# Kernel tuning notes

Hardware: AMD Instinct MI355X
Metric: run time of the kernel (lower is better)

Reference implementation:

```python
import jax, jax.numpy as jnp
import numpy as np

B = 128      # number of swarms
NA = 64      # agents per swarm (na)
D = 8        # input feature dim
RD = 128     # attention hidden dim r
H = 16       # output channels h (l = sqrt(h) = 4)


def setup_inputs() -> dict:
    key = jax.random.key(0)
    ks = jax.random.split(key, 16)
    x = jax.random.normal(ks[0], (B * NA, D, NA), dtype=jnp.float32)
    L = jax.random.randint(ks[1], (B * NA, D, NA), 0, 2).astype(jnp.float32)
    p = lambda k, shp: jax.random.normal(k, shp, dtype=jnp.float32)
    return {
        "x": x, "L": L,
        "Aq": p(ks[2], (RD, D)), "Ak": p(ks[3], (RD, D)), "Av": p(ks[4], (RD, D)),
        "Aq1": p(ks[5], (RD, RD)), "Ak1": p(ks[6], (RD, RD)), "Av1": p(ks[7], (RD, RD)),
        "Aq5": p(ks[8], (RD, RD)), "Ak5": p(ks[9], (RD, RD)), "Av5": p(ks[10], (RD, RD)),
        "Ao": p(ks[11], (RD, RD)), "Ao1": p(ks[12], (RD, RD)), "Ao5": p(ks[13], (H, RD)),
    }


def _attn(Xin, Aq, Ak, Av, sqrt_nn):
    # Xin: (b, f, n); Aq/Ak/Av: (r, f); sqrt_nn: (b, 1, 1)
    Q = jax.nn.sigmoid(jnp.einsum('rf,bfn->bnr', Aq, Xin))   # Q already transposed
    K = jax.nn.sigmoid(jnp.einsum('rf,bfn->brn', Ak, Xin))
    V = jax.nn.sigmoid(jnp.einsum('rf,bfn->bnr', Av, Xin))
    S = jnp.einsum('bnr,brm->bnm', Q, K) / sqrt_nn           # (b, n, n)
    A = jax.nn.softmax(S, axis=2)
    return jnp.einsum('bnm,bmr->brn', A, V)                  # o^T: (b, r, n)


def _kron_eye2(A):
    # torch.kron(A, eye(2)) per batch: (B, n, n) -> (B, 2n, 2n)
    Bq, n, _ = A.shape
    I2 = jnp.eye(2, dtype=A.dtype)
    return (A[:, :, None, :, None] * I2[None, :, None, :]).reshape(Bq, 2 * n, 2 * n)


def reference(x, L, Aq, Ak, Av, Aq1, Ak1, Av1, Aq5, Ak5, Av5, Ao, Ao1, Ao5):
    na = x.shape[2]
    Bsw = x.shape[0] // na
    num_nb = jnp.sum((L[:, 0, :] >= 1.0).astype(jnp.float32), axis=1) + 1.0
    sqrt_nn = jnp.sqrt(num_nb)[:, None, None]                # (Bx, 1, 1)

    o = _attn(x, Aq, Ak, Av, sqrt_nn)
    R = jax.nn.silu(jnp.einsum('sr,brn->bsn', Ao, o))
    o = _attn(R, Aq1, Ak1, Av1, sqrt_nn)
    R = jax.nn.silu(jnp.einsum('sr,brn->bsn', Ao1, o))
    o = _attn(R, Aq5, Ak5, Av5, sqrt_nn)
    R = jax.nn.silu(jnp.einsum('hr,brn->bhn', Ao5, o))       # (Bx, 16, na)

    blk = lambda a, b: R[:, a:b, :].sum(axis=1).reshape(Bsw, na, na)
    R11 = _kron_eye2(blk(0, 4))
    R12 = _kron_eye2(blk(4, 8))
    R21 = _kron_eye2(blk(8, 12))
    R22 = _kron_eye2(blk(12, 16))
    # block matrix [[R11, R12], [R21, R22]] -> (Bsw, 4na, 4na)
    Rfull = jnp.concatenate(
        (jnp.concatenate((R11, R21), axis=1), jnp.concatenate((R12, R22), axis=1)),
        axis=2)

    Rfull = Rfull ** 2
    Rupper = Rfull + jnp.swapaxes(Rfull, 1, 2)
    n_tot = 4 * na
    Dg = jnp.eye(n_tot, dtype=Rupper.dtype)
    Rdiag = Rupper * (1.0 - Dg)                              # diag zeroed
    Rout = Dg * Rupper                                       # keep diag only
    rowsum = jnp.sum(Rdiag, axis=2)[:, :, None]              # (Bsw, n, 1)
    return Rout + Dg * rowsum - Rdiag
```

## Files before the change

kernel.cpp:

```cpp
#include <hip/hip_runtime.h>
#include <hip/hip_bf16.h>

typedef _Float16 f16;
typedef __attribute__((ext_vector_type(8))) _Float16 h8v;
typedef __attribute__((ext_vector_type(4))) float f4v;
typedef __attribute__((ext_vector_type(16))) float f16acc;

#define OFF_WQ  0
#define OFF_WK  2048
#define OFF_WV  4096
#define OFF_AQ1 6144
#define OFF_AK1 22528
#define OFF_AV1 38912
#define OFF_AQ5 55296
#define OFF_AK5 71680
#define OFF_AV5 88064
#define OFF_AO  104448
#define OFF_AO1 120832
#define OFF_AO5 137216
#define WTS_TOTAL 139264

__device__ __forceinline__ f4v mfma16_(h8v a, h8v b, f4v c) {
  return __builtin_amdgcn_mfma_f32_16x16x32_f16(a, b, c, 0, 0, 0);
}
__device__ __forceinline__ f16acc mfma32_(h8v a, h8v b, f16acc c) {
  return __builtin_amdgcn_mfma_f32_32x32x16_f16(a, b, c, 0, 0, 0);
}
__device__ __forceinline__ float rcp_(float x) { return __builtin_amdgcn_rcpf(x); }
__device__ __forceinline__ unsigned int pk2(float a, float b) {
  __fp16 __attribute__((ext_vector_type(2))) h2 = __builtin_amdgcn_cvt_pkrtz(a, b);
  return *reinterpret_cast<unsigned int*>(&h2);
}
__device__ __forceinline__ f16acc zero16() {
  f16acc z;
  #pragma unroll
  for (int i = 0; i < 16; ++i) z[i] = 0.f;
  return z;
}

__device__ __forceinline__ f16* swz256(f16* b, int n, int k) {
  int byte = (n << 8) + (k << 1); byte ^= (n & 7) << 4;
  return (f16*)((char*)b + byte);
}
__device__ __forceinline__ const f16* swz256c(const f16* b, int n, int k) {
  int byte = (n << 8) + (k << 1); byte ^= (n & 7) << 4;
  return (const f16*)((const char*)b + byte);
}
__device__ __forceinline__ f16* swz128(f16* b, int r, int m) {
  int byte = (r << 7) + (m << 1); byte ^= (r & 7) << 4;
  return (f16*)((char*)b + byte);
}
__device__ __forceinline__ const f16* swz128c(const f16* b, int r, int m) {
  int byte = (r << 7) + (m << 1); byte ^= (r & 7) << 4;
  return (const f16*)((const char*)b + byte);
}

template<int ACT>
__device__ __forceinline__ unsigned long long pack4act(f4v acc) {
  float v[4];
  #pragma unroll
  for (int j = 0; j < 4; ++j) {
    float t = acc[j];
    if (ACT == 0)      t = rcp_(1.0f + __expf(-t));
    else if (ACT == 1) t = t * rcp_(1.0f + __expf(-t));
    v[j] = t;
  }
  union { unsigned long long u64; unsigned int u32[2]; } u;
  u.u32[0] = pk2(v[0], v[1]);
  u.u32[1] = pk2(v[2], v[3]);
  return u.u64;
}

template<int NKK>
__device__ __forceinline__ void mm_qkv(const f16* __restrict__ Wq,
                                       const f16* __restrict__ Wk,
                                       const f16* __restrict__ Wv,
                                       const f16* __restrict__ Xt,
                                       f16* __restrict__ Qt, f16* __restrict__ Kt,
                                       f16* __restrict__ Vb, int w, int lane)
{
  const int l31 = lane & 31, lh = lane >> 5;
  const int rt = w >> 1, ct = w & 1;
  h8v xf[NKK];
  #pragma unroll
  for (int kk = 0; kk < NKK; ++kk)
    xf[kk] = *(const h8v*)swz256c(Xt, ct * 32 + l31, kk * 16 + lh * 8);
  f16acc aq = zero16(), ak = zero16(), av = zero16();
  #pragma unroll
  for (int kk = 0; kk < NKK; ++kk) {
    const int fo = (rt * NKK + kk) * 512 + lane * 8;
    h8v fq = *(const h8v*)(Wq + fo);
    h8v fk = *(const h8v*)(Wk + fo);
    h8v fv = *(const h8v*)(Wv + fo);
    aq = mfma32_(fq, xf[kk], aq);
    ak = mfma32_(fk, xf[kk], ak);
    av = mfma32_(xf[kk], fv, av);
  }
  const int n = ct * 32 + l31;
  #pragma unroll
  for (int q = 0; q < 4; ++q) {
    const int rr = rt * 32 + q * 8 + lh * 4;
    f4v t;
    t = (f4v){aq[4*q], aq[4*q+1], aq[4*q+2], aq[4*q+3]};
    *(unsigned long long*)swz256(Qt, n, rr) = pack4act<0>(t);
    t = (f4v){ak[4*q], ak[4*q+1], ak[4*q+2], ak[4*q+3]};
    *(unsigned long long*)swz256(Kt, n, rr) = pack4act<0>(t);
    t = (f4v){av[4*q], av[4*q+1], av[4*q+2], av[4*q+3]};
    *(unsigned long long*)swz128(Vb, rt * 32 + l31, ct * 32 + q * 8 + lh * 4) = pack4act<0>(t);
  }
}

__device__ __forceinline__ void mm_pv32(const f16* __restrict__ Vb,
                                        const f16* __restrict__ Ps,
                                        f16* __restrict__ Ot, int w, int lane)
{
  const int l31 = lane & 31, lh = lane >> 5;
  const int rt = w >> 1, ct = w & 1;
  f16acc acc = zero16();
  #pragma unroll
  for (int kk = 0; kk < 4; ++kk) {
    h8v a = *(const h8v*)swz128c(Vb, rt * 32 + l31, kk * 16 + lh * 8);
    h8v b = *(const h8v*)swz128c(Ps, ct * 32 + l31, kk * 16 + lh * 8);
    acc = mfma32_(a, b, acc);
  }
  const int n = ct * 32 + l31;
  #pragma unroll
  for (int q = 0; q < 4; ++q) {
    f4v t = (f4v){acc[4*q], acc[4*q+1], acc[4*q+2], acc[4*q+3]};
    *(unsigned long long*)swz256(Ot, n, rt * 32 + q * 8 + lh * 4) = pack4act<2>(t);
  }
}

__device__ __forceinline__ void mm_ao32(const f16* __restrict__ Ao,
                                        const f16* __restrict__ Ot,
                                        f16* __restrict__ Rt, int w, int lane)
{
  const int l31 = lane & 31, lh = lane >> 5;
  const int st = w >> 1, ct = w & 1;
  f16acc acc = zero16();
  #pragma unroll
  for (int kk = 0; kk < 8; ++kk) {
    h8v a = *(const h8v*)(Ao + (st * 8 + kk) * 512 + lane * 8);
    h8v b = *(const h8v*)swz256c(Ot, ct * 32 + l31, kk * 16 + lh * 8);
    acc = mfma32_(a, b, acc);
  }
  const int n = ct * 32 + l31;
  #pragma unroll
  for (int q = 0; q < 4; ++q) {
    f4v t = (f4v){acc[4*q], acc[4*q+1], acc[4*q+2], acc[4*q+3]};
    *(unsigned long long*)swz256(Rt, n, st * 32 + q * 8 + lh * 4) = pack4act<1>(t);
  }
}

__device__ __forceinline__ void s_softmax(const f16* __restrict__ QtL,
                                          const f16* __restrict__ KtL,
                                          f16* __restrict__ PsL,
                                          float is, int w, int lane)
{
  const int lrow = lane & 15, lk = lane >> 4;
  const int n = 16 * w + lrow;
  h8v bq[4];
  #pragma unroll
  for (int kk = 0; kk < 4; ++kk)
    bq[kk] = *(const h8v*)swz256c(QtL, n, kk * 32 + lk * 8);
  f4v acc[4];
  #pragma unroll
  for (int mt = 0; mt < 4; ++mt) {
    acc[mt] = (f4v){0.f, 0.f, 0.f, 0.f};
    #pragma unroll
    for (int kk = 0; kk < 4; ++kk) {
      h8v ak = *(const h8v*)swz256c(KtL, mt * 16 + lrow, kk * 32 + lk * 8);
      acc[mt] = mfma16_(ak, bq[kk], acc[mt]);
    }
  }
  float mx = -1e30f;
  #pragma unroll
  for (int mt = 0; mt < 4; ++mt)
    #pragma unroll
    for (int j = 0; j < 4; ++j) { acc[mt][j] *= is; mx = fmaxf(mx, acc[mt][j]); }
  mx = fmaxf(mx, __shfl_xor(mx, 16));
  mx = fmaxf(mx, __shfl_xor(mx, 32));
  float sm = 0.f;
  #pragma unroll
  for (int mt = 0; mt < 4; ++mt)
    #pragma unroll
    for (int j = 0; j < 4; ++j) { acc[mt][j] = __expf(acc[mt][j] - mx); sm += acc[mt][j]; }
  sm += __shfl_xor(sm, 16);
  sm += __shfl_xor(sm, 32);
  const float inv = rcp_(sm);
  #pragma unroll
  for (int mt = 0; mt < 4; ++mt) {
    union { unsigned long long u64; unsigned int u32[2]; } u;
    u.u32[0] = pk2(acc[mt][0] * inv, acc[mt][1] * inv);
    u.u32[1] = pk2(acc[mt][2] * inv, acc[mt][3] * inv);
    *(unsigned long long*)swz128(PsL, n, mt * 16 + lk * 4) = u.u64;
  }
}

__device__ __forceinline__ void mm_final(const f16* __restrict__ Ao5g,
                                         const f16* __restrict__ OtL,
                                         float* __restrict__ rch_b, int w, int lane)
{
  const int lrow = lane & 15, lk = lane >> 4;
  h8v a[4];
  #pragma unroll
  for (int kk = 0; kk < 4; ++kk)
    a[kk] = *(const h8v*)(Ao5g + lrow * 128 + kk * 32 + lk * 8);
  const int n = 16 * w + lrow;
  f4v acc = {0.f, 0.f, 0.f, 0.f};
  #pragma unroll
  for (int kk = 0; kk < 4; ++kk) {
    h8v b = *(const h8v*)swz256c(OtL, n, kk * 32 + lk * 8);
    acc = mfma16_(a[kk], b, acc);
  }
  #pragma unroll
  for (int j = 0; j < 4; ++j) {
    float v = acc[j];
    v = v * rcp_(1.0f + __expf(-v));
    rch_b[(lk * 4 + j) * 64 + n] = v;
  }
}

__global__ __launch_bounds__(512, 4)
void swarm_attn_mfma(const float* __restrict__ x, const float* __restrict__ L,
                     const f16* __restrict__ wts, float* __restrict__ rch)
{
  __shared__ f16 Xt[64 * 128];
  __shared__ f16 Qt[64 * 128];
  __shared__ f16 Kt[64 * 128];
  __shared__ f16 Vb[128 * 64];
  __shared__ f16 Ps[64 * 64];
  __shared__ float s_inv;

  const int b = blockIdx.x;
  const int tid = threadIdx.x;
  const int w = tid >> 6, lane = tid & 63;

  {
    const int n = tid >> 3, c = tid & 7;
    unsigned int val = 0;
    if (c < 4) {
      const float a  = x[(size_t)b * 512 + (2 * c) * 64 + n];
      const float bb = x[(size_t)b * 512 + (2 * c + 1) * 64 + n];
      val = pk2(a, bb);
    }
    *(unsigned int*)swz256(Xt, n, 2 * c) = val;
  }
  if (w == 0) {
    const float lv = L[(size_t)b * 512 + lane];
    const unsigned long long msk = __ballot(lv >= 1.0f);
    if (lane == 0) s_inv = __frsqrt_rn((float)(__popcll(msk) + 1));
  }
  __syncthreads();
  const float is = s_inv;

  mm_qkv<1>(wts + OFF_WQ, wts + OFF_WK, wts + OFF_WV, Xt, Qt, Kt, Vb, w, lane);
  __syncthreads();
  if (w < 4) s_softmax(Qt, Kt, Ps, is, w, lane);
  __syncthreads();
  mm_pv32(Vb, Ps, Qt, w, lane);
  __syncthreads();
  mm_ao32(wts + OFF_AO, Qt, Xt, w, lane);
  __syncthreads();

  mm_qkv<8>(wts + OFF_AQ1, wts + OFF_AK1, wts + OFF_AV1, Xt, Qt, Kt, Vb, w, lane);
  __syncthreads();
  if (w < 4) s_softmax(Qt, Kt, Ps, is, w, lane);
  __syncthreads();
  mm_pv32(Vb, Ps, Qt, w, lane);
  __syncthreads();
  mm_ao32(wts + OFF_AO1, Qt, Xt, w, lane);
  __syncthreads();

  mm_qkv<8>(wts + OFF_AQ5, wts + OFF_AK5, wts + OFF_AV5, Xt, Qt, Kt, Vb, w, lane);
  __syncthreads();
  if (w < 4) s_softmax(Qt, Kt, Ps, is, w, lane);
  __syncthreads();
  mm_pv32(Vb, Ps, Qt, w, lane);
  __syncthreads();
  if (w < 4) mm_final(wts + OFF_AO5, Qt, rch + (size_t)b * 1024, w, lane);
}

__global__ void conv_wts(const float* Aq, const float* Ak, const float* Av,
                         const float* Aq1, const float* Ak1, const float* Av1,
                         const float* Aq5, const float* Ak5, const float* Av5,
                         const float* Ao, const float* Ao1, const float* Ao5,
                         f16* wts)
{
  const int t = blockIdx.x * 256 + threadIdx.x;
  if (t >= WTS_TOTAL) return;
  float v;
  if (t < 6144) {
    const int m = t >> 11, idx = t & 2047;
    const int fi = idx >> 9, rem = idx & 511, lane = rem >> 3, j = rem & 7;
    const int r = fi * 32 + (lane & 31), k = (lane >> 5) * 8 + j;
    const float* W = (m == 0) ? Aq : (m == 1) ? Ak : Av;
    v = (k < 8) ? W[r * 8 + k] : 0.f;
  } else if (t < 137216) {
    const int m = (t - 6144) >> 14, idx = (t - 6144) & 16383;
    const int fi = idx >> 9, rem = idx & 511, lane = rem >> 3, j = rem & 7;
    const int rt = fi >> 3, kk = fi & 7;
    const int r = rt * 32 + (lane & 31), k = kk * 16 + (lane >> 5) * 8 + j;
    const float* W = (m == 0) ? Aq1 : (m == 1) ? Ak1 : (m == 2) ? Av1 :
                     (m == 3) ? Aq5 : (m == 4) ? Ak5 : (m == 5) ? Av5 :
                     (m == 6) ? Ao : Ao1;
    v = W[r * 128 + k];
  } else {
    v = Ao5[t - 137216];
  }
  wts[t] = (f16)v;
}

#define ASTR 65
__global__ __launch_bounds__(256, 1)
void reduce_kernel(const float* __restrict__ rch, float* __restrict__ Mw,
                   float* __restrict__ rsw, float* __restrict__ csw)
{
  __shared__ float Msh[4 * 64 * ASTR];
  const int s = blockIdx.x, t = threadIdx.x;
  for (int e = t; e < 16384; e += 256) {
    const int j = e & 63, i = (e >> 6) & 63, g = e >> 12;
    const float* p = rch + ((size_t)s * 64 + i) * 1024 + (4 * g) * 64 + j;
    const float v = p[0] + p[64] + p[128] + p[192];
    Msh[(g * 64 + i) * ASTR + j] = v;
    Mw[(size_t)s * 16384 + e] = v;
  }
  __syncthreads();
  const int g = t >> 6, i = t & 63;
  float r2 = 0.f, c2 = 0.f;
  for (int j = 0; j < 64; ++j) {
    const float a = Msh[(g * 64 + i) * ASTR + j];
    const float bb = Msh[(g * 64 + j) * ASTR + i];
    r2 = fmaf(a, a, r2);
    c2 = fmaf(bb, bb, c2);
  }
  rsw[s * 256 + g * 64 + i] = r2;
  csw[s * 256 + g * 64 + i] = c2;
}

__global__ __launch_bounds__(256, 1)
void expand_kernel(const float* __restrict__ Mw, const float* __restrict__ rsw,
                   const float* __restrict__ csw, float* __restrict__ out)
{
  const size_t e = ((size_t)blockIdx.x * 256 + threadIdx.x) * 4;
  const int s = (int)(e >> 16);
  const int rem = (int)(e & 65535);
  const int u = rem >> 8, v0 = rem & 255;
  const int ub = u >> 7, ii = (u & 127) >> 1, p = u & 1;
  const float* Ms = Mw + (size_t)s * 16384;
  float4 o;
  float* po = &o.x;
  #pragma unroll
  for (int c = 0; c < 4; ++c) {
    const int v = v0 + c;
    const int vb = v >> 7, jj = (v & 127) >> 1, q = v & 1;
    float val = 0.f;
    if (u == v) {
      val = rsw[s * 256 + (2 * ub) * 64 + ii] + rsw[s * 256 + (2 * ub + 1) * 64 + ii]
          + csw[s * 256 + ub * 64 + ii] + csw[s * 256 + (2 + ub) * 64 + ii];
    } else if (p == q) {
      const int g = 2 * ub + vb, gp = 2 * vb + ub;
      const float a = Ms[g * 4096 + ii * 64 + jj];
      const float bb = Ms[gp * 4096 + jj * 64 + ii];
      val = -(a * a + bb * bb);
    }
    po[c] = val;
  }
  *(float4*)(out + e) = o;
}

extern "C" void kernel_launch(void* const* d_in, const int* in_sizes, int n_in,
                              void* d_out, int out_size, void* d_ws, size_t ws_size,
                              hipStream_t stream)
{
  const float* x   = (const float*)d_in[0];
  const float* L   = (const float*)d_in[1];
  const float* Aq  = (const float*)d_in[2];
  const float* Ak  = (const float*)d_in[3];
  const float* Av  = (const float*)d_in[4];
  const float* Aq1 = (const float*)d_in[5];
  const float* Ak1 = (const float*)d_in[6];
  const float* Av1 = (const float*)d_in[7];
  const float* Aq5 = (const float*)d_in[8];
  const float* Ak5 = (const float*)d_in[9];
  const float* Av5 = (const float*)d_in[10];
  const float* Ao  = (const float*)d_in[11];
  const float* Ao1 = (const float*)d_in[12];
  const float* Ao5 = (const float*)d_in[13];

  f16* wts = (f16*)d_ws;
  float* Mw  = (float*)((char*)d_ws + (size_t)WTS_TOTAL * 2);
  float* rsw = Mw + (size_t)128 * 16384;
  float* csw = rsw + 128 * 256;
  float* rch = (float*)d_out;

  conv_wts<<<(WTS_TOTAL + 255) / 256, 256, 0, stream>>>(Aq, Ak, Av, Aq1, Ak1, Av1,
                                                        Aq5, Ak5, Av5, Ao, Ao1, Ao5, wts);
  swarm_attn_mfma<<<8192, 512, 0, stream>>>(x, L, wts, rch);
  reduce_kernel<<<128, 256, 0, stream>>>(rch, Mw, rsw, csw);
  expand_kernel<<<8192, 256, 0, stream>>>(Mw, rsw, csw, (float*)d_out);
}
```

Before: 332.2 us.

## Keep per-wave activations in registers with 16x16x16 MFMA tiling

Restructures the attention kernel so each of 4 waves owns 16 agents and keeps Q, P, O and the next-layer input in registers as 16x16x16 MFMA fragments. Only K and V go through shared memory, which removes the Xt/Qt/Ps buffers and about half the barriers per layer. Weights are repacked for the new fragment layout. In exchange it uses the older 16x16x16 MFMA with half the K depth, issues more MFMA instructions, and runs 256-thread blocks with higher register pressure.

After: 573.2 us. 1.73x slower.

```diff
diff --git a/kernel.cpp b/kernel.cpp
--- a/kernel.cpp
+++ b/kernel.cpp
@@ -1,10 +1,9 @@
 #include <hip/hip_runtime.h>
-#include <hip/hip_bf16.h>
 
 typedef _Float16 f16;
+typedef __attribute__((ext_vector_type(4))) _Float16 h4v;
 typedef __attribute__((ext_vector_type(8))) _Float16 h8v;
 typedef __attribute__((ext_vector_type(4))) float f4v;
-typedef __attribute__((ext_vector_type(16))) float f16acc;
 
 #define OFF_WQ  0
 #define OFF_WK  2048
@@ -20,23 +19,14 @@
 #define OFF_AO5 137216
 #define WTS_TOTAL 139264
 
-__device__ __forceinline__ f4v mfma16_(h8v a, h8v b, f4v c) {
-  return __builtin_amdgcn_mfma_f32_16x16x32_f16(a, b, c, 0, 0, 0);
-}
-__device__ __forceinline__ f16acc mfma32_(h8v a, h8v b, f16acc c) {
-  return __builtin_amdgcn_mfma_f32_32x32x16_f16(a, b, c, 0, 0, 0);
+__device__ __forceinline__ f4v mfma_(h4v a, h4v b, f4v c) {
+  return __builtin_amdgcn_mfma_f32_16x16x16f16(a, b, c, 0, 0, 0);
 }
 __device__ __forceinline__ float rcp_(float x) { return __builtin_amdgcn_rcpf(x); }
 __device__ __forceinline__ unsigned int pk2(float a, float b) {
   __fp16 __attribute__((ext_vector_type(2))) h2 = __builtin_amdgcn_cvt_pkrtz(a, b);
   return *reinterpret_cast<unsigned int*>(&h2);
 }
-__device__ __forceinline__ f16acc zero16() {
-  f16acc z;
-  #pragma unroll
-  for (int i = 0; i < 16; ++i) z[i] = 0.f;
-  return z;
-}
 
 __device__ __forceinline__ f16* swz256(f16* b, int n, int k) {
   int byte = (n << 8) + (k << 1); byte ^= (n & 7) << 4;
@@ -55,8 +45,10 @@
   return (const f16*)((const char*)b + byte);
 }
 
+union pkun { unsigned long long u64; unsigned int u32[2]; h4v h; };
+
 template<int ACT>
-__device__ __forceinline__ unsigned long long pack4act(f4v acc) {
+__device__ __forceinline__ pkun pack4act(f4v acc) {
   float v[4];
   #pragma unroll
   for (int j = 0; j < 4; ++j) {
@@ -65,112 +57,67 @@
     else if (ACT == 1) t = t * rcp_(1.0f + __expf(-t));
     v[j] = t;
   }
-  union { unsigned long long u64; unsigned int u32[2]; } u;
+  pkun u;
   u.u32[0] = pk2(v[0], v[1]);
   u.u32[1] = pk2(v[2], v[3]);
-  return u.u64;
-}
-
-template<int NKK>
-__device__ __forceinline__ void mm_qkv(const f16* __restrict__ Wq,
-                                       const f16* __restrict__ Wk,
-                                       const f16* __restrict__ Wv,
-                                       const f16* __restrict__ Xt,
-                                       f16* __restrict__ Qt, f16* __restrict__ Kt,
-                                       f16* __restrict__ Vb, int w, int lane)
-{
-  const int l31 = lane & 31, lh = lane >> 5;
-  const int rt = w >> 1, ct = w & 1;
-  h8v xf[NKK];
-  #pragma unroll
-  for (int kk = 0; kk < NKK; ++kk)
-    xf[kk] = *(const h8v*)swz256c(Xt, ct * 32 + l31, kk * 16 + lh * 8);
-  f16acc aq = zero16(), ak = zero16(), av = zero16();
-  #pragma unroll
-  for (int kk = 0; kk < NKK; ++kk) {
-    const int fo = (rt * NKK + kk) * 512 + lane * 8;
-    h8v fq = *(const h8v*)(Wq + fo);
-    h8v fk = *(const h8v*)(Wk + fo);
-    h8v fv = *(const h8v*)(Wv + fo);
-    aq = mfma32_(fq, xf[kk], aq);
-    ak = mfma32_(fk, xf[kk], ak);
-    av = mfma32_(xf[kk], fv, av);
-  }
-  const int n = ct * 32 + l31;
-  #pragma unroll
-  for (int q = 0; q < 4; ++q) {
-    const int rr = rt * 32 + q * 8 + lh * 4;
-    f4v t;
-    t = (f4v){aq[4*q], aq[4*q+1], aq[4*q+2], aq[4*q+3]};
-    *(unsigned long long*)swz256(Qt, n, rr) = pack4act<0>(t);
-    t = (f4v){ak[4*q], ak[4*q+1], ak[4*q+2], ak[4*q+3]};
-    *(unsigned long long*)swz256(Kt, n, rr) = pack4act<0>(t);
-    t = (f4v){av[4*q], av[4*q+1], av[4*q+2], av[4*q+3]};
-    *(unsigned long long*)swz128(Vb, rt * 32 + l31, ct * 32 + q * 8 + lh * 4) = pack4act<0>(t);
-  }
-}
-
-__device__ __forceinline__ void mm_pv32(const f16* __restrict__ Vb,
-                                        const f16* __restrict__ Ps,
-                                        f16* __restrict__ Ot, int w, int lane)
-{
-  const int l31 = lane & 31, lh = lane >> 5;
-  const int rt = w >> 1, ct = w & 1;
-  f16acc acc = zero16();
-  #pragma unroll
-  for (int kk = 0; kk < 4; ++kk) {
-    h8v a = *(const h8v*)swz128c(Vb, rt * 32 + l31, kk * 16 + lh * 8);
-    h8v b = *(const h8v*)swz128c(Ps, ct * 32 + l31, kk * 16 + lh * 8);
-    acc = mfma32_(a, b, acc);
-  }
-  const int n = ct * 32 + l31;
-  #pragma unroll
-  for (int q = 0; q < 4; ++q) {
-    f4v t = (f4v){acc[4*q], acc[4*q+1], acc[4*q+2], acc[4*q+3]};
-    *(unsigned long long*)swz256(Ot, n, rt * 32 + q * 8 + lh * 4) = pack4act<2>(t);
-  }
-}
-
-__device__ __forceinline__ void mm_ao32(const f16* __restrict__ Ao,
-                                        const f16* __restrict__ Ot,
-                                        f16* __restrict__ Rt, int w, int lane)
-{
-  const int l31 = lane & 31, lh = lane >> 5;
-  const int st = w >> 1, ct = w & 1;
-  f16acc acc = zero16();
-  #pragma unroll
-  for (int kk = 0; kk < 8; ++kk) {
-    h8v a = *(const h8v*)(Ao + (st * 8 + kk) * 512 + lane * 8);
-    h8v b = *(const h8v*)swz256c(Ot, ct * 32 + l31, kk * 16 + lh * 8);
-    acc = mfma32_(a, b, acc);
-  }
-  const int n = ct * 32 + l31;
-  #pragma unroll
-  for (int q = 0; q < 4; ++q) {
-    f4v t = (f4v){acc[4*q], acc[4*q+1], acc[4*q+2], acc[4*q+3]};
-    *(unsigned long long*)swz256(Rt, n, st * 32 + q * 8 + lh * 4) = pack4act<1>(t);
-  }
-}
-
-__device__ __forceinline__ void s_softmax(const f16* __restrict__ QtL,
-                                          const f16* __restrict__ KtL,
-                                          f16* __restrict__ PsL,
-                                          float is, int w, int lane)
-{
-  const int lrow = lane & 15, lk = lane >> 4;
-  const int n = 16 * w + lrow;
-  h8v bq[4];
-  #pragma unroll
-  for (int kk = 0; kk < 4; ++kk)
-    bq[kk] = *(const h8v*)swz256c(QtL, n, kk * 32 + lk * 8);
+  return u;
+}
+
+__device__ __forceinline__ h4v lo4(h8v p) { return __builtin_shufflevector(p, p, 0, 1, 2, 3); }
+__device__ __forceinline__ h4v hi4(h8v p) { return __builtin_shufflevector(p, p, 4, 5, 6, 7); }
+
+template<int NF>
+__device__ __forceinline__ void qkv_phase(const f16* __restrict__ Wq,
+                                          const f16* __restrict__ Wk,
+                                          const f16* __restrict__ Wv,
+                                          const h4v* __restrict__ xf,
+                                          h4v* __restrict__ qreg,
+                                          f16* __restrict__ Kt, f16* __restrict__ Vb,
+                                          int lane, int n, int lrow, int lk, int s0)
+{
+  #pragma unroll
+  for (int rt = 0; rt < 8; ++rt) {
+    f4v aq = {0.f,0.f,0.f,0.f}, ak = {0.f,0.f,0.f,0.f}, av = {0.f,0.f,0.f,0.f};
+    if (NF == 1) {
+      h4v fq = *(const h4v*)(Wq + rt * 256 + lane * 4);
+      h4v fk = *(const h4v*)(Wk + rt * 256 + lane * 4);
+      h4v fv = *(const h4v*)(Wv + rt * 256 + lane * 4);
+      aq = mfma_(fq, xf[0], aq);
+      ak = mfma_(fk, xf[0], ak);
+      av = mfma_(xf[0], fv, av);
+    } else {
+      #pragma unroll
+      for (int kp = 0; kp < NF / 2; ++kp) {
+        h8v pq = *(const h8v*)(Wq + (rt * 4 + kp) * 512 + lane * 8);
+        h8v pk = *(const h8v*)(Wk + (rt * 4 + kp) * 512 + lane * 8);
+        h8v pv = *(const h8v*)(Wv + (rt * 4 + kp) * 512 + lane * 8);
+        aq = mfma_(lo4(pq), xf[2 * kp], aq);
+        aq = mfma_(hi4(pq), xf[2 * kp + 1], aq);
+        ak = mfma_(lo4(pk), xf[2 * kp], ak);
+        ak = mfma_(hi4(pk), xf[2 * kp + 1], ak);
+        av = mfma_(xf[2 * kp], lo4(pv), av);
+        av = mfma_(xf[2 * kp + 1], hi4(pv), av);
+      }
+    }
+    qreg[rt] = pack4act<0>(aq).h;
+    *(unsigned long long*)swz256(Kt, n, rt * 16 + lk * 4) = pack4act<0>(ak).u64;
+    *(unsigned long long*)swz128(Vb, rt * 16 + lrow, s0 + lk * 4) = pack4act<0>(av).u64;
+  }
+}
+
+__device__ __forceinline__ void softmax_phase(const f16* __restrict__ Kt,
+                                              const h4v* __restrict__ qreg,
+                                              h4v* __restrict__ preg,
+                                              float is, int lrow, int lk)
+{
   f4v acc[4];
   #pragma unroll
   for (int mt = 0; mt < 4; ++mt) {
     acc[mt] = (f4v){0.f, 0.f, 0.f, 0.f};
     #pragma unroll
-    for (int kk = 0; kk < 4; ++kk) {
-      h8v ak = *(const h8v*)swz256c(KtL, mt * 16 + lrow, kk * 32 + lk * 8);
-      acc[mt] = mfma16_(ak, bq[kk], acc[mt]);
+    for (int kr = 0; kr < 8; ++kr) {
+      h4v a = *(const h4v*)swz256c(Kt, mt * 16 + lrow, kr * 16 + lk * 4);
+      acc[mt] = mfma_(a, qreg[kr], acc[mt]);
     }
   }
   float mx = -1e30f;
@@ -190,95 +137,108 @@
   const float inv = rcp_(sm);
   #pragma unroll
   for (int mt = 0; mt < 4; ++mt) {
-    union { unsigned long long u64; unsigned int u32[2]; } u;
+    pkun u;
     u.u32[0] = pk2(acc[mt][0] * inv, acc[mt][1] * inv);
     u.u32[1] = pk2(acc[mt][2] * inv, acc[mt][3] * inv);
-    *(unsigned long long*)swz128(PsL, n, mt * 16 + lk * 4) = u.u64;
-  }
-}
-
-__device__ __forceinline__ void mm_final(const f16* __restrict__ Ao5g,
-                                         const f16* __restrict__ OtL,
-                                         float* __restrict__ rch_b, int w, int lane)
-{
-  const int lrow = lane & 15, lk = lane >> 4;
-  h8v a[4];
-  #pragma unroll
-  for (int kk = 0; kk < 4; ++kk)
-    a[kk] = *(const h8v*)(Ao5g + lrow * 128 + kk * 32 + lk * 8);
-  const int n = 16 * w + lrow;
-  f4v acc = {0.f, 0.f, 0.f, 0.f};
-  #pragma unroll
-  for (int kk = 0; kk < 4; ++kk) {
-    h8v b = *(const h8v*)swz256c(OtL, n, kk * 32 + lk * 8);
-    acc = mfma16_(a[kk], b, acc);
-  }
-  #pragma unroll
-  for (int j = 0; j < 4; ++j) {
-    float v = acc[j];
-    v = v * rcp_(1.0f + __expf(-v));
-    rch_b[(lk * 4 + j) * 64 + n] = v;
-  }
-}
-
-__global__ __launch_bounds__(512, 4)
+    preg[mt] = u.h;
+  }
+}
+
+__device__ __forceinline__ void pv_phase(const f16* __restrict__ Vb,
+                                         const h4v* __restrict__ preg,
+                                         h4v* __restrict__ oreg, int lrow, int lk)
+{
+  #pragma unroll
+  for (int rt = 0; rt < 8; ++rt) {
+    f4v acc = {0.f, 0.f, 0.f, 0.f};
+    #pragma unroll
+    for (int km = 0; km < 4; ++km) {
+      h4v a = *(const h4v*)swz128c(Vb, rt * 16 + lrow, km * 16 + lk * 4);
+      acc = mfma_(a, preg[km], acc);
+    }
+    oreg[rt] = pack4act<2>(acc).h;
+  }
+}
+
+__device__ __forceinline__ void ao_phase(const f16* __restrict__ Ao,
+                                         const h4v* __restrict__ oreg,
+                                         h4v* __restrict__ xf, int lane)
+{
+  #pragma unroll
+  for (int st = 0; st < 8; ++st) {
+    f4v acc = {0.f, 0.f, 0.f, 0.f};
+    #pragma unroll
+    for (int kp = 0; kp < 4; ++kp) {
+      h8v pa = *(const h8v*)(Ao + (st * 4 + kp) * 512 + lane * 8);
+      acc = mfma_(lo4(pa), oreg[2 * kp], acc);
+      acc = mfma_(hi4(pa), oreg[2 * kp + 1], acc);
+    }
+    xf[st] = pack4act<1>(acc).h;
+  }
+}
+
+__global__ __launch_bounds__(256, 4)
 void swarm_attn_mfma(const float* __restrict__ x, const float* __restrict__ L,
                      const f16* __restrict__ wts, float* __restrict__ rch)
 {
-  __shared__ f16 Xt[64 * 128];
-  __shared__ f16 Qt[64 * 128];
   __shared__ f16 Kt[64 * 128];
   __shared__ f16 Vb[128 * 64];
-  __shared__ f16 Ps[64 * 64];
   __shared__ float s_inv;
 
-  const int b = blockIdx.x;
-  const int tid = threadIdx.x;
+  const int b = blockIdx.x, tid = threadIdx.x;
   const int w = tid >> 6, lane = tid & 63;
+  const int lrow = lane & 15, lk = lane >> 4;
+  const int s0 = w * 16;
+  const int n = s0 + lrow;
+
+  h4v xf[8], qreg[8], preg[4], oreg[8];
+
+  #pragma unroll
+  for (int j = 0; j < 4; ++j) {
+    const int f = lk * 4 + j;
+    xf[0][j] = (f < 8) ? (f16)x[(size_t)b * 512 + f * 64 + n] : (f16)0.f;
+  }
+  if (tid < 64) {
+    const float lv = L[(size_t)b * 512 + tid];
+    const unsigned long long msk = __ballot(lv >= 1.0f);
+    if (tid == 0) s_inv = __frsqrt_rn((float)(__popcll(msk) + 1));
+  }
+
+  qkv_phase<1>(wts + OFF_WQ, wts + OFF_WK, wts + OFF_WV, xf, qreg, Kt, Vb, lane, n, lrow, lk, s0);
+  __syncthreads();
+  const float is = s_inv;
+  softmax_phase(Kt, qreg, preg, is, lrow, lk);
+  pv_phase(Vb, preg, oreg, lrow, lk);
+  __syncthreads();
+  ao_phase(wts + OFF_AO, oreg, xf, lane);
+
+  qkv_phase<8>(wts + OFF_AQ1, wts + OFF_AK1, wts + OFF_AV1, xf, qreg, Kt, Vb, lane, n, lrow, lk, s0);
+  __syncthreads();
+  softmax_phase(Kt, qreg, preg, is, lrow, lk);
+  pv_phase(Vb, preg, oreg, lrow, lk);
+  __syncthreads();
+  ao_phase(wts + OFF_AO1, oreg, xf, lane);
+
+  qkv_phase<8>(wts + OFF_AQ5, wts + OFF_AK5, wts + OFF_AV5, xf, qreg, Kt, Vb, lane, n, lrow, lk, s0);
+  __syncthreads();
+  softmax_phase(Kt, qreg, preg, is, lrow, lk);
+  pv_phase(Vb, preg, oreg, lrow, lk);
 
   {
-    const int n = tid >> 3, c = tid & 7;
-    unsigned int val = 0;
-    if (c < 4) {
-      const float a  = x[(size_t)b * 512 + (2 * c) * 64 + n];
-      const float bb = x[(size_t)b * 512 + (2 * c + 1) * 64 + n];
-      val = pk2(a, bb);
-    }
-    *(unsigned int*)swz256(Xt, n, 2 * c) = val;
-  }
-  if (w == 0) {
-    const float lv = L[(size_t)b * 512 + lane];
-    const unsigned long long msk = __ballot(lv >= 1.0f);
-    if (lane == 0) s_inv = __frsqrt_rn((float)(__popcll(msk) + 1));
-  }
-  __syncthreads();
-  const float is = s_inv;
-
-  mm_qkv<1>(wts + OFF_WQ, wts + OFF_WK, wts + OFF_WV, Xt, Qt, Kt, Vb, w, lane);
-  __syncthreads();
-  if (w < 4) s_softmax(Qt, Kt, Ps, is, w, lane);
-  __syncthreads();
-  mm_pv32(Vb, Ps, Qt, w, lane);
-  __syncthreads();
-  mm_ao32(wts + OFF_AO, Qt, Xt, w, lane);
-  __syncthreads();
-
-  mm_qkv<8>(wts + OFF_AQ1, wts + OFF_AK1, wts + OFF_AV1, Xt, Qt, Kt, Vb, w, lane);
-  __syncthreads();
-  if (w < 4) s_softmax(Qt, Kt, Ps, is, w, lane);
-  __syncthreads();
-  mm_pv32(Vb, Ps, Qt, w, lane);
-  __syncthreads();
-  mm_ao32(wts + OFF_AO1, Qt, Xt, w, lane);
-  __syncthreads();
-
-  mm_qkv<8>(wts + OFF_AQ5, wts + OFF_AK5, wts + OFF_AV5, Xt, Qt, Kt, Vb, w, lane);
-  __syncthreads();
-  if (w < 4) s_softmax(Qt, Kt, Ps, is, w, lane);
-  __syncthreads();
-  mm_pv32(Vb, Ps, Qt, w, lane);
-  __syncthreads();
-  if (w < 4) mm_final(wts + OFF_AO5, Qt, rch + (size_t)b * 1024, w, lane);
+    f4v acc = {0.f, 0.f, 0.f, 0.f};
+    #pragma unroll
+    for (int kp = 0; kp < 4; ++kp) {
+      h8v pa = *(const h8v*)(wts + OFF_AO5 + kp * 512 + lane * 8);
+      acc = mfma_(lo4(pa), oreg[2 * kp], acc);
+      acc = mfma_(hi4(pa), oreg[2 * kp + 1], acc);
+    }
+    #pragma unroll
+    for (int j = 0; j < 4; ++j) {
+      float v = acc[j];
+      v = v * rcp_(1.0f + __expf(-v));
+      rch[(size_t)b * 1024 + (lk * 4 + j) * 64 + n] = v;
+    }
+  }
 }
 
 __global__ void conv_wts(const float* Aq, const float* Ak, const float* Av,
@@ -292,21 +252,27 @@
   float v;
   if (t < 6144) {
     const int m = t >> 11, idx = t & 2047;
-    const int fi = idx >> 9, rem = idx & 511, lane = rem >> 3, j = rem & 7;
-    const int r = fi * 32 + (lane & 31), k = (lane >> 5) * 8 + j;
+    const int fi = idx >> 8, rem = idx & 255, lane = rem >> 2, j = rem & 3;
+    const int r = fi * 16 + (lane & 15), k = (lane >> 4) * 4 + j;
     const float* W = (m == 0) ? Aq : (m == 1) ? Ak : Av;
     v = (k < 8) ? W[r * 8 + k] : 0.f;
   } else if (t < 137216) {
     const int m = (t - 6144) >> 14, idx = (t - 6144) & 16383;
-    const int fi = idx >> 9, rem = idx & 511, lane = rem >> 3, j = rem & 7;
-    const int rt = fi >> 3, kk = fi & 7;
-    const int r = rt * 32 + (lane & 31), k = kk * 16 + (lane >> 5) * 8 + j;
+    const int c = idx >> 9, rem = idx & 511, lane = rem >> 3, sub = rem & 7;
+    const int half = sub >> 2, j = sub & 3;
+    const int rt = c >> 2, kk = (c & 3) * 2 + half;
+    const int r = rt * 16 + (lane & 15), k = kk * 16 + (lane >> 4) * 4 + j;
     const float* W = (m == 0) ? Aq1 : (m == 1) ? Ak1 : (m == 2) ? Av1 :
                      (m == 3) ? Aq5 : (m == 4) ? Ak5 : (m == 5) ? Av5 :
                      (m == 6) ? Ao : Ao1;
     v = W[r * 128 + k];
   } else {
-    v = Ao5[t - 137216];
+    const int idx = t - 137216;
+    const int c = idx >> 9, rem = idx & 511, lane = rem >> 3, sub = rem & 7;
+    const int half = sub >> 2, j = sub & 3;
+    const int kk = c * 2 + half;
+    const int r = lane & 15, k = kk * 16 + (lane >> 4) * 4 + j;
+    v = Ao5[r * 128 + k];
   }
   wts[t] = (f16)v;
 }
@@ -396,7 +362,7 @@
 
   conv_wts<<<(WTS_TOTAL + 255) / 256, 256, 0, stream>>>(Aq, Ak, Av, Aq1, Ak1, Av1,
                                                         Aq5, Ak5, Av5, Ao, Ao1, Ao5, wts);
-  swarm_attn_mfma<<<8192, 512, 0, stream>>>(x, L, wts, rch);
+  swarm_attn_mfma<<<8192, 256, 0, stream>>>(x, L, wts, rch);
   reduce_kernel<<<128, 256, 0, stream>>>(rch, Mw, rsw, csw);
   expand_kernel<<<8192, 256, 0, stream>>>(Mw, rsw, csw, (float*)d_out);
 }
```

## Replace XOR swizzle with padded LDS rows and split softmax across all warps

Applied to the files above, without the earlier changes.

Shared-memory tiles switch from XOR-swizzled addressing to padded row strides (136 and 72 halves), which simplifies address arithmetic while still avoiding bank conflicts. The softmax stage now uses all 8 warps, each covering half the key columns, with cross-warp max and sum exchanged through small shared arrays and two extra barriers. Ps is aliased onto Xt to keep LDS usage in check despite the padding. The cost is extra synchronization inside softmax and a slightly larger LDS footprint, which could affect occupancy at 4 blocks per CU.

Measured after the change: 335.9 us. No clear change (+1.1%).

```diff
diff --git a/kernel.cpp b/kernel.cpp
--- a/kernel.cpp
+++ b/kernel.cpp
@@ -1,5 +1,4 @@
 #include <hip/hip_runtime.h>
-#include <hip/hip_bf16.h>
 
 typedef _Float16 f16;
 typedef __attribute__((ext_vector_type(8))) _Float16 h8v;
@@ -20,6 +19,9 @@
 #define OFF_AO5 137216
 #define WTS_TOTAL 139264
 
+#define P2 136
+#define P1 72
+
 __device__ __forceinline__ f4v mfma16_(h8v a, h8v b, f4v c) {
   return __builtin_amdgcn_mfma_f32_16x16x32_f16(a, b, c, 0, 0, 0);
 }
@@ -38,29 +40,12 @@
   return z;
 }
 
-__device__ __forceinline__ f16* swz256(f16* b, int n, int k) {
-  int byte = (n << 8) + (k << 1); byte ^= (n & 7) << 4;
-  return (f16*)((char*)b + byte);
-}
-__device__ __forceinline__ const f16* swz256c(const f16* b, int n, int k) {
-  int byte = (n << 8) + (k << 1); byte ^= (n & 7) << 4;
-  return (const f16*)((const char*)b + byte);
-}
-__device__ __forceinline__ f16* swz128(f16* b, int r, int m) {
-  int byte = (r << 7) + (m << 1); byte ^= (r & 7) << 4;
-  return (f16*)((char*)b + byte);
-}
-__device__ __forceinline__ const f16* swz128c(const f16* b, int r, int m) {
-  int byte = (r << 7) + (m << 1); byte ^= (r & 7) << 4;
-  return (const f16*)((const char*)b + byte);
-}
-
 template<int ACT>
-__device__ __forceinline__ unsigned long long pack4act(f4v acc) {
-  float v[4];
+__device__ __forceinline__ unsigned long long pack4act(float a, float b, float c, float d) {
+  float v[4] = {a, b, c, d};
   #pragma unroll
   for (int j = 0; j < 4; ++j) {
-    float t = acc[j];
+    float t = v[j];
     if (ACT == 0)      t = rcp_(1.0f + __expf(-t));
     else if (ACT == 1) t = t * rcp_(1.0f + __expf(-t));
     v[j] = t;
@@ -72,7 +57,7 @@
 }
 
 template<int NKK>
-__device__ __forceinline__ void mm_qkv(const f16* __restrict__ Wq,
+__device__ __forceinline__ void qkv_ph(const f16* __restrict__ Wq,
                                        const f16* __restrict__ Wk,
                                        const f16* __restrict__ Wv,
                                        const f16* __restrict__ Xt,
@@ -81,10 +66,11 @@
 {
   const int l31 = lane & 31, lh = lane >> 5;
   const int rt = w >> 1, ct = w & 1;
+  const int xbase = (ct * 32 + l31) * P2 + lh * 8;
   h8v xf[NKK];
   #pragma unroll
   for (int kk = 0; kk < NKK; ++kk)
-    xf[kk] = *(const h8v*)swz256c(Xt, ct * 32 + l31, kk * 16 + lh * 8);
+    xf[kk] = *(const h8v*)(Xt + xbase + kk * 16);
   f16acc aq = zero16(), ak = zero16(), av = zero16();
   #pragma unroll
   for (int kk = 0; kk < NKK; ++kk) {
@@ -96,44 +82,98 @@
     ak = mfma32_(fk, xf[kk], ak);
     av = mfma32_(xf[kk], fv, av);
   }
-  const int n = ct * 32 + l31;
+  const int nrow = (ct * 32 + l31) * P2;
+  const int vrow = (rt * 32 + l31) * P1 + ct * 32 + lh * 4;
   #pragma unroll
   for (int q = 0; q < 4; ++q) {
     const int rr = rt * 32 + q * 8 + lh * 4;
-    f4v t;
-    t = (f4v){aq[4*q], aq[4*q+1], aq[4*q+2], aq[4*q+3]};
-    *(unsigned long long*)swz256(Qt, n, rr) = pack4act<0>(t);
-    t = (f4v){ak[4*q], ak[4*q+1], ak[4*q+2], ak[4*q+3]};
-    *(unsigned long long*)swz256(Kt, n, rr) = pack4act<0>(t);
-    t = (f4v){av[4*q], av[4*q+1], av[4*q+2], av[4*q+3]};
-    *(unsigned long long*)swz128(Vb, rt * 32 + l31, ct * 32 + q * 8 + lh * 4) = pack4act<0>(t);
-  }
-}
-
-__device__ __forceinline__ void mm_pv32(const f16* __restrict__ Vb,
-                                        const f16* __restrict__ Ps,
-                                        f16* __restrict__ Ot, int w, int lane)
+    *(unsigned long long*)(Qt + nrow + rr) =
+        pack4act<0>(aq[4*q], aq[4*q+1], aq[4*q+2], aq[4*q+3]);
+    *(unsigned long long*)(Kt + nrow + rr) =
+        pack4act<0>(ak[4*q], ak[4*q+1], ak[4*q+2], ak[4*q+3]);
+    *(unsigned long long*)(Vb + vrow + q * 8) =
+        pack4act<0>(av[4*q], av[4*q+1], av[4*q+2], av[4*q+3]);
+  }
+}
+
+__device__ __forceinline__ void softmax_ph(const f16* __restrict__ Qt,
+                                           const f16* __restrict__ Kt,
+                                           f16* __restrict__ Ps,
+                                           float* __restrict__ smax,
+                                           float* __restrict__ ssum,
+                                           float is, int w, int lane)
+{
+  const int lrow = lane & 15, lk = lane >> 4;
+  const int nst = w & 3, mh = w >> 2;
+  const int n = nst * 16 + lrow;
+  h8v bq[4];
+  #pragma unroll
+  for (int kk = 0; kk < 4; ++kk)
+    bq[kk] = *(const h8v*)(Qt + n * P2 + kk * 32 + lk * 8);
+  f4v acc[2];
+  #pragma unroll
+  for (int t = 0; t < 2; ++t) {
+    const int mt = mh * 2 + t;
+    acc[t] = (f4v){0.f, 0.f, 0.f, 0.f};
+    #pragma unroll
+    for (int kk = 0; kk < 4; ++kk) {
+      h8v a = *(const h8v*)(Kt + (mt * 16 + lrow) * P2 + kk * 32 + lk * 8);
+      acc[t] = mfma16_(a, bq[kk], acc[t]);
+    }
+  }
+  float mx = -1e30f;
+  #pragma unroll
+  for (int t = 0; t < 2; ++t)
+    #pragma unroll
+    for (int j = 0; j < 4; ++j) { acc[t][j] *= is; mx = fmaxf(mx, acc[t][j]); }
+  mx = fmaxf(mx, __shfl_xor(mx, 16));
+  mx = fmaxf(mx, __shfl_xor(mx, 32));
+  if (lk == 0) smax[mh * 64 + n] = mx;
+  __syncthreads();
+  const float gmax = fmaxf(smax[n], smax[64 + n]);
+  float sm = 0.f;
+  #pragma unroll
+  for (int t = 0; t < 2; ++t)
+    #pragma unroll
+    for (int j = 0; j < 4; ++j) { acc[t][j] = __expf(acc[t][j] - gmax); sm += acc[t][j]; }
+  sm += __shfl_xor(sm, 16);
+  sm += __shfl_xor(sm, 32);
+  if (lk == 0) ssum[mh * 64 + n] = sm;
+  __syncthreads();
+  const float inv = rcp_(ssum[n] + ssum[64 + n]);
+  #pragma unroll
+  for (int t = 0; t < 2; ++t) {
+    const int mt = mh * 2 + t;
+    union { unsigned long long u64; unsigned int u32[2]; } u;
+    u.u32[0] = pk2(acc[t][0] * inv, acc[t][1] * inv);
+    u.u32[1] = pk2(acc[t][2] * inv, acc[t][3] * inv);
+    *(unsigned long long*)(Ps + n * P1 + mt * 16 + lk * 4) = u.u64;
+  }
+}
+
+__device__ __forceinline__ void pv_ph(const f16* __restrict__ Vb,
+                                      const f16* __restrict__ Ps,
+                                      f16* __restrict__ Ot, int w, int lane)
 {
   const int l31 = lane & 31, lh = lane >> 5;
   const int rt = w >> 1, ct = w & 1;
   f16acc acc = zero16();
   #pragma unroll
   for (int kk = 0; kk < 4; ++kk) {
-    h8v a = *(const h8v*)swz128c(Vb, rt * 32 + l31, kk * 16 + lh * 8);
-    h8v b = *(const h8v*)swz128c(Ps, ct * 32 + l31, kk * 16 + lh * 8);
+    h8v a = *(const h8v*)(Vb + (rt * 32 + l31) * P1 + kk * 16 + lh * 8);
+    h8v b = *(const h8v*)(Ps + (ct * 32 + l31) * P1 + kk * 16 + lh * 8);
     acc = mfma32_(a, b, acc);
   }
-  const int n = ct * 32 + l31;
-  #pragma unroll
-  for (int q = 0; q < 4; ++q) {
-    f4v t = (f4v){acc[4*q], acc[4*q+1], acc[4*q+2], acc[4*q+3]};
-    *(unsigned long long*)swz256(Ot, n, rt * 32 + q * 8 + lh * 4) = pack4act<2>(t);
-  }
-}
-
-__device__ __forceinline__ void mm_ao32(const f16* __restrict__ Ao,
-                                        const f16* __restrict__ Ot,
-                                        f16* __restrict__ Rt, int w, int lane)
+  const int nrow = (ct * 32 + l31) * P2;
+  #pragma unroll
+  for (int q = 0; q < 4; ++q)
+    *(unsigned long long*)(Ot + nrow + rt * 32 + q * 8 + lh * 4) =
+        pack4act<2>(acc[4*q], acc[4*q+1], acc[4*q+2], acc[4*q+3]);
+}
+
+__device__ __forceinline__ void ao_ph(const f16* __restrict__ Ao,
+                                      const f16* __restrict__ Ot,
+                                      f16* __restrict__ Rt, int w, int lane)
 {
   const int l31 = lane & 31, lh = lane >> 5;
   const int st = w >> 1, ct = w & 1;
@@ -141,64 +181,18 @@
   #pragma unroll
   for (int kk = 0; kk < 8; ++kk) {
     h8v a = *(const h8v*)(Ao + (st * 8 + kk) * 512 + lane * 8);
-    h8v b = *(const h8v*)swz256c(Ot, ct * 32 + l31, kk * 16 + lh * 8);
+    h8v b = *(const h8v*)(Ot + (ct * 32 + l31) * P2 + kk * 16 + lh * 8);
     acc = mfma32_(a, b, acc);
   }
-  const int n = ct * 32 + l31;
-  #pragma unroll
-  for (int q = 0; q < 4; ++q) {
-    f4v t = (f4v){acc[4*q], acc[4*q+1], acc[4*q+2], acc[4*q+3]};
-    *(unsigned long long*)swz256(Rt, n, st * 32 + q * 8 + lh * 4) = pack4act<1>(t);
-  }
-}
-
-__device__ __forceinline__ void s_softmax(const f16* __restrict__ QtL,
-                                          const f16* __restrict__ KtL,
-                                          f16* __restrict__ PsL,
-                                          float is, int w, int lane)
-{
-  const int lrow = lane & 15, lk = lane >> 4;
-  const int n = 16 * w + lrow;
-  h8v bq[4];
-  #pragma unroll
-  for (int kk = 0; kk < 4; ++kk)
-    bq[kk] = *(const h8v*)swz256c(QtL, n, kk * 32 + lk * 8);
-  f4v acc[4];
-  #pragma unroll
-  for (int mt = 0; mt < 4; ++mt) {
-    acc[mt] = (f4v){0.f, 0.f, 0.f, 0.f};
-    #pragma unroll
-    for (int kk = 0; kk < 4; ++kk) {
-      h8v ak = *(const h8v*)swz256c(KtL, mt * 16 + lrow, kk * 32 + lk * 8);
-      acc[mt] = mfma16_(ak, bq[kk], acc[mt]);
-    }
-  }
-  float mx = -1e30f;
-  #pragma unroll
-  for (int mt = 0; mt < 4; ++mt)
-    #pragma unroll
-    for (int j = 0; j < 4; ++j) { acc[mt][j] *= is; mx = fmaxf(mx, acc[mt][j]); }
-  mx = fmaxf(mx, __shfl_xor(mx, 16));
-  mx = fmaxf(mx, __shfl_xor(mx, 32));
-  float sm = 0.f;
-  #pragma unroll
-  for (int mt = 0; mt < 4; ++mt)
-    #pragma unroll
-    for (int j = 0; j < 4; ++j) { acc[mt][j] = __expf(acc[mt][j] - mx); sm += acc[mt][j]; }
-  sm += __shfl_xor(sm, 16);
-  sm += __shfl_xor(sm, 32);
-  const float inv = rcp_(sm);
-  #pragma unroll
-  for (int mt = 0; mt < 4; ++mt) {
-    union { unsigned long long u64; unsigned int u32[2]; } u;
-    u.u32[0] = pk2(acc[mt][0] * inv, acc[mt][1] * inv);
-    u.u32[1] = pk2(acc[mt][2] * inv, acc[mt][3] * inv);
-    *(unsigned long long*)swz128(PsL, n, mt * 16 + lk * 4) = u.u64;
-  }
-}
-
-__device__ __forceinline__ void mm_final(const f16* __restrict__ Ao5g,
-                                         const f16* __restrict__ OtL,
+  const int nrow = (ct * 32 + l31) * P2;
+  #pragma unroll
+  for (int q = 0; q < 4; ++q)
+    *(unsigned long long*)(Rt + nrow + st * 32 + q * 8 + lh * 4) =
+        pack4act<1>(acc[4*q], acc[4*q+1], acc[4*q+2], acc[4*q+3]);
+}
+
+__device__ __forceinline__ void final_ph(const f16* __restrict__ Ao5g,
+                                         const f16* __restrict__ Ot,
                                          float* __restrict__ rch_b, int w, int lane)
 {
   const int lrow = lane & 15, lk = lane >> 4;
@@ -210,7 +204,7 @@
   f4v acc = {0.f, 0.f, 0.f, 0.f};
   #pragma unroll
   for (int kk = 0; kk < 4; ++kk) {
-    h8v b = *(const h8v*)swz256c(OtL, n, kk * 32 + lk * 8);
+    h8v b = *(const h8v*)(Ot + n * P2 + kk * 32 + lk * 8);
     acc = mfma16_(a[kk], b, acc);
   }
   #pragma unroll
@@ -225,12 +219,14 @@
 void swarm_attn_mfma(const float* __restrict__ x, const float* __restrict__ L,
                      const f16* __restrict__ wts, float* __restrict__ rch)
 {
-  __shared__ f16 Xt[64 * 128];
-  __shared__ f16 Qt[64 * 128];
-  __shared__ f16 Kt[64 * 128];
-  __shared__ f16 Vb[128 * 64];
-  __shared__ f16 Ps[64 * 64];
+  __shared__ f16 Xt[64 * P2];
+  __shared__ f16 Qt[64 * P2];
+  __shared__ f16 Kt[64 * P2];
+  __shared__ f16 Vb[128 * P1];
+  __shared__ float smax[2 * 64];
+  __shared__ float ssum[2 * 64];
   __shared__ float s_inv;
+  f16* Ps = Xt;
 
   const int b = blockIdx.x;
   const int tid = threadIdx.x;
@@ -244,7 +240,7 @@
       const float bb = x[(size_t)b * 512 + (2 * c + 1) * 64 + n];
       val = pk2(a, bb);
     }
-    *(unsigned int*)swz256(Xt, n, 2 * c) = val;
+    *(unsigned int*)(Xt + n * P2 + 2 * c) = val;
   }
   if (w == 0) {
     const float lv = L[(size_t)b * 512 + lane];
@@ -254,31 +250,31 @@
   __syncthreads();
   const float is = s_inv;
 
-  mm_qkv<1>(wts + OFF_WQ, wts + OFF_WK, wts + OFF_WV, Xt, Qt, Kt, Vb, w, lane);
-  __syncthreads();
-  if (w < 4) s_softmax(Qt, Kt, Ps, is, w, lane);
-  __syncthreads();
-  mm_pv32(Vb, Ps, Qt, w, lane);
-  __syncthreads();
-  mm_ao32(wts + OFF_AO, Qt, Xt, w, lane);
-  __syncthreads();
-
-  mm_qkv<8>(wts + OFF_AQ1, wts + OFF_AK1, wts + OFF_AV1, Xt, Qt, Kt, Vb, w, lane);
-  __syncthreads();
-  if (w < 4) s_softmax(Qt, Kt, Ps, is, w, lane);
-  __syncthreads();
-  mm_pv32(Vb, Ps, Qt, w, lane);
-  __syncthreads();
-  mm_ao32(wts + OFF_AO1, Qt, Xt, w, lane);
-  __syncthreads();
-
-  mm_qkv<8>(wts + OFF_AQ5, wts + OFF_AK5, wts + OFF_AV5, Xt, Qt, Kt, Vb, w, lane);
-  __syncthreads();
-  if (w < 4) s_softmax(Qt, Kt, Ps, is, w, lane);
-  __syncthreads();
-  mm_pv32(Vb, Ps, Qt, w, lane);
-  __syncthreads();
-  if (w < 4) mm_final(wts + OFF_AO5, Qt, rch + (size_t)b * 1024, w, lane);
+  qkv_ph<1>(wts + OFF_WQ, wts + OFF_WK, wts + OFF_WV, Xt, Qt, Kt, Vb, w, lane);
+  __syncthreads();
+  softmax_ph(Qt, Kt, Ps, smax, ssum, is, w, lane);
+  __syncthreads();
+  pv_ph(Vb, Ps, Qt, w, lane);
+  __syncthreads();
+  ao_ph(wts + OFF_AO, Qt, Xt, w, lane);
+  __syncthreads();
+
+  qkv_ph<8>(wts + OFF_AQ1, wts + OFF_AK1, wts + OFF_AV1, Xt, Qt, Kt, Vb, w, lane);
+  __syncthreads();
+  softmax_ph(Qt, Kt, Ps, smax, ssum, is, w, lane);
+  __syncthreads();
+  pv_ph(Vb, Ps, Qt, w, lane);
+  __syncthreads();
+  ao_ph(wts + OFF_AO1, Qt, Xt, w, lane);
+  __syncthreads();
+
+  qkv_ph<8>(wts + OFF_AQ5, wts + OFF_AK5, wts + OFF_AV5, Xt, Qt, Kt, Vb, w, lane);
+  __syncthreads();
+  softmax_ph(Qt, Kt, Ps, smax, ssum, is, w, lane);
+  __syncthreads();
+  pv_ph(Vb, Ps, Qt, w, lane);
+  __syncthreads();
+  if (w < 4) final_ph(wts + OFF_AO5, Qt, rch + (size_t)b * 1024, w, lane);
 }
 
 __global__ void conv_wts(const float* Aq, const float* Ak, const float* Av,
```
